# Optimization experiments

Hardware: AMD Instinct MI355X
Metric: run time of the kernel (lower is better)

The kernel has to match this reference:

```python
import jax, jax.numpy as jnp
import numpy as np
import math

B, N = 1, 512
C_S, C_Z, C_H, H, L, RECYCLE = 384, 128, 16, 12, 8, 2


def setup_inputs():
    key = jax.random.key(0)
    ks = jax.random.split(key, 16)
    w = lambda k, shape: jax.random.normal(k, shape, dtype=jnp.float32) * 0.02
    return {
        's': jax.random.normal(ks[0], (B, N, C_S), jnp.float32),
        'z': jax.random.normal(ks[1], (B, N, N, C_Z), jnp.float32),
        'Wq': w(ks[2], (L, C_S, H * C_H)), 'bq': jnp.zeros((L, H * C_H), jnp.float32),
        'Wk': w(ks[3], (L, C_S, H * C_H)), 'bk': jnp.zeros((L, H * C_H), jnp.float32),
        'Wv': w(ks[4], (L, C_S, H * C_H)), 'bv': jnp.zeros((L, H * C_H), jnp.float32),
        'Wb': w(ks[5], (L, C_Z, H)), 'bb': jnp.zeros((L, H), jnp.float32),
        'Wo': w(ks[6], (L, H * (C_H + C_Z), C_S)), 'bo': jnp.zeros((L, C_S), jnp.float32),
        'Wt1': w(ks[7], (L, C_S, 4 * C_S)), 'bt1': jnp.zeros((L, 4 * C_S), jnp.float32),
        'Wt2': w(ks[8], (L, 4 * C_S, C_S)), 'bt2': jnp.zeros((L, C_S), jnp.float32),
        'Wu': w(ks[9], (L, C_S, 6)), 'bu': jnp.zeros((L, 6), jnp.float32),
        'ln_g': jnp.ones((2 * L, C_S), jnp.float32),
        'ln_b': jnp.zeros((2 * L, C_S), jnp.float32),
    }


def _layer_norm(x, g, b, eps=1e-5):
    mu = jnp.mean(x, axis=-1, keepdims=True)
    var = jnp.mean((x - mu) ** 2, axis=-1, keepdims=True)
    return (x - mu) / jnp.sqrt(var + eps) * g + b


def _forward(s, z, Wq, bq, Wk, bk, Wv, bv, Wb, bb, Wo, bo, Wt1, bt1, Wt2, bt2, Wu, bu, ln_g, ln_b):
    b_, n_, _ = s.shape
    coords = jnp.zeros((b_, n_, 3), s.dtype)
    inv_sqrt_c = 1.0 / math.sqrt(C_H)
    for _r in range(RECYCLE):
        for i in range(L):
            # ---- Invariant Point Attention ----
            q = (s @ Wq[i] + bq[i]).reshape(b_, n_, H, C_H)
            k = (s @ Wk[i] + bk[i]).reshape(b_, n_, H, C_H)
            v = (s @ Wv[i] + bv[i]).reshape(b_, n_, H, C_H)
            attn = jnp.einsum('bihc,bjhc->bijh', q, k) * inv_sqrt_c  # (B,N,N,H)
            bias_z = z @ Wb[i] + bb[i]  # (B,N,N,H)
            # multiscale cdist bias: <=5A -> 1.0, <=15A -> 0.3, else 0.05
            sq = jnp.sum((coords[:, :, None, :] - coords[:, None, :, :]) ** 2, axis=-1)
            d = jnp.sqrt(jnp.maximum(sq, 1e-12))
            ms = jnp.where(d <= 5.0, 1.0, jnp.where(d <= 15.0, 0.3, 0.05))[..., None]
            attn = attn + bias_z + ms
            wgt = jax.nn.softmax(attn, axis=2)  # softmax over j
            scalar = jnp.einsum('bijh,bjhc->bihc', wgt, v)
            pair = jnp.einsum('bijh,bijc->bihc', wgt, z)
            o = jnp.concatenate([scalar, pair], axis=-1).reshape(b_, n_, H * (C_H + C_Z))
            s = _layer_norm(s + (o @ Wo[i] + bo[i]), ln_g[2 * i], ln_b[2 * i])
            # ---- Transition (FFN) ----
            t = jax.nn.relu(s @ Wt1[i] + bt1[i]) @ Wt2[i] + bt2[i]
            s = _layer_norm(s + t, ln_g[2 * i + 1], ln_b[2 * i + 1])
            # ---- Backbone update: source discards quaternion, applies translation only ----
            upd = s @ Wu[i] + bu[i]
            coords = coords + upd[..., :3]
    return coords


def reference(s, z, Wq, bq, Wk, bk, Wv, bv, Wb, bb, Wo, bo, Wt1, bt1, Wt2, bt2, Wu, bu, ln_g, ln_b):
    return _forward(s, z, Wq, bq, Wk, bk, Wv, bv, Wb, bb, Wo, bo, Wt1, bt1, Wt2, bt2, Wu, bu, ln_g, ln_b)
```

## Files before the change

### kernel.cpp

```cpp
#include <hip/hip_runtime.h>


constexpr int N    = 512;
constexpr int CS   = 384;
constexpr int CZ   = 128;
constexpr int CH   = 16;
constexpr int H    = 12;
constexpr int L    = 8;
constexpr int RECY = 2;
constexpr int HCH  = H * CH;
constexpr int QKVN = 3 * HCH;
constexpr int OD   = H * (CH + CZ);
constexpr int FF   = 4 * CS;
constexpr int MB   = 96;
constexpr long long NN2 = (long long)N * N;

typedef __bf16 bf16x8 __attribute__((ext_vector_type(8)));
typedef float  f32x4  __attribute__((ext_vector_type(4)));
typedef unsigned short us8 __attribute__((ext_vector_type(8)));

__device__ __forceinline__ ushort f2bf(float f) {
    uint u = __builtin_bit_cast(uint, f);
    return (ushort)((u + 0x7fffu + ((u >> 16) & 1u)) >> 16);
}
__device__ __forceinline__ float bf2f(ushort h) {
    uint u = ((uint)h) << 16;
    return __builtin_bit_cast(float, u);
}

__global__ __launch_bounds__(256) void init_s(
    const float* __restrict__ s_in, float* __restrict__ scur, ushort* __restrict__ sbf)
{
    int i = blockIdx.x * 256 + threadIdx.x;
    float v = s_in[i];
    scur[i] = v;
    sbf[i]  = f2bf(v);
}

__global__ __launch_bounds__(256) void pack_bqkv(
    const float* __restrict__ bq, const float* __restrict__ bk,
    const float* __restrict__ bv, float* __restrict__ bqkv)
{
    int idx = blockIdx.x * 256 + threadIdx.x;
    if (idx >= L * QKVN) return;
    int n = idx % QKVN, l = idx / QKVN;
    int sel = n / HCH, nn = n % HCH;
    const float* bp = sel == 0 ? bq : (sel == 1 ? bk : bv);
    bqkv[idx] = bp[l * HCH + nn];
}

__global__ __launch_bounds__(256) void pack_qkv_t(
    const float* __restrict__ Wq, const float* __restrict__ Wk,
    const float* __restrict__ Wv, ushort* __restrict__ WqkvT)
{
    __shared__ float tile[32][33];
    const int l = blockIdx.z;
    const int k0 = blockIdx.x * 32, n0 = blockIdx.y * 32;
    const int tx = threadIdx.x & 31, ty = threadIdx.x >> 5;
    const int sel = n0 / HCH;
    const int nn0 = n0 - sel * HCH;
    const float* W = sel == 0 ? Wq : (sel == 1 ? Wk : Wv);
    #pragma unroll
    for (int r = 0; r < 32; r += 8)
        tile[ty + r][tx] = W[((size_t)l * CS + k0 + ty + r) * HCH + nn0 + tx];
    __syncthreads();
    #pragma unroll
    for (int r = 0; r < 32; r += 8)
        WqkvT[((size_t)l * QKVN + n0 + ty + r) * CS + k0 + tx] = f2bf(tile[tx][ty + r]);
}

__global__ __launch_bounds__(256) void transpose_w(
    const float* __restrict__ in, ushort* __restrict__ out, int K, int Nn)
{
    __shared__ float tile[32][33];
    const int l = blockIdx.z;
    const float* ip = in + (size_t)l * K * Nn;
    ushort* op = out + (size_t)l * K * Nn;
    const int k0 = blockIdx.x * 32, n0 = blockIdx.y * 32;
    const int tx = threadIdx.x & 31, ty = threadIdx.x >> 5;
    #pragma unroll
    for (int r = 0; r < 32; r += 8)
        tile[ty + r][tx] = ip[(size_t)(k0 + ty + r) * Nn + n0 + tx];
    __syncthreads();
    #pragma unroll
    for (int r = 0; r < 32; r += 8)
        op[(size_t)(n0 + ty + r) * K + k0 + tx] = f2bf(tile[tx][ty + r]);
}

__global__ __launch_bounds__(256) void pack_wbt(
    const float* __restrict__ Wb, ushort* __restrict__ WbT)
{
    int idx = blockIdx.x * 256 + threadIdx.x;
    int m = idx >> 7, c = idx & 127;
    int l = m / H, h = m % H;
    WbT[idx] = f2bf(Wb[((size_t)l * CZ + c) * H + h]);
}

__global__ __launch_bounds__(256) void bias_gemm(
    const ushort* __restrict__ WbT, const float* __restrict__ z,
    const float* __restrict__ bb, ushort* __restrict__ bias_all)
{
    const int w = threadIdx.x >> 6, lane = threadIdx.x & 63;
    const int lm = lane & 15, kg = lane >> 4;
    const size_t ij0 = (size_t)blockIdx.x * 256 + (size_t)w * 64;
    __shared__ float bbs[MB];
    if (threadIdx.x < MB) bbs[threadIdx.x] = bb[threadIdx.x];
    __syncthreads();
    f32x4 acc[6][4];
    #pragma unroll
    for (int mt = 0; mt < 6; mt++)
        #pragma unroll
        for (int nt = 0; nt < 4; nt++) acc[mt][nt] = (f32x4){0.f, 0.f, 0.f, 0.f};
    #pragma unroll
    for (int kc = 0; kc < 4; kc++) {
        const int k = kc * 32 + kg * 8;
        bf16x8 b[4];
        #pragma unroll
        for (int nt = 0; nt < 4; nt++) {
            const float* zp = z + (ij0 + nt * 16 + lm) * CZ + k;
            float4 z0 = *(const float4*)zp, z1 = *(const float4*)(zp + 4);
            b[nt][0] = (__bf16)z0.x; b[nt][1] = (__bf16)z0.y;
            b[nt][2] = (__bf16)z0.z; b[nt][3] = (__bf16)z0.w;
            b[nt][4] = (__bf16)z1.x; b[nt][5] = (__bf16)z1.y;
            b[nt][6] = (__bf16)z1.z; b[nt][7] = (__bf16)z1.w;
        }
        #pragma unroll
        for (int mt = 0; mt < 6; mt++) {
            bf16x8 a = *(const bf16x8*)(WbT + (size_t)(mt * 16 + lm) * CZ + k);
            #pragma unroll
            for (int nt = 0; nt < 4; nt++)
                acc[mt][nt] = __builtin_amdgcn_mfma_f32_16x16x32_bf16(a, b[nt], acc[mt][nt], 0, 0, 0);
        }
    }
    #pragma unroll
    for (int mt = 0; mt < 6; mt++)
        #pragma unroll
        for (int nt = 0; nt < 4; nt++)
            #pragma unroll
            for (int r = 0; r < 4; r++) {
                int m = mt * 16 + kg * 4 + r;
                bias_all[(size_t)m * NN2 + ij0 + nt * 16 + lm] = f2bf(acc[mt][nt][r] + bbs[m]);
            }
}

__global__ __launch_bounds__(256) void gemm_bf16(
    const ushort* __restrict__ A, const ushort* __restrict__ Bt,
    const float* __restrict__ bias, float* __restrict__ C, ushort* __restrict__ Cbf,
    int M, int Nn, int K, int kper, int relu)
{
    const int w = threadIdx.x >> 6, lane = threadIdx.x & 63;
    const int lm = lane & 15, kg = lane >> 4;
    const int m0 = blockIdx.y * 64 + w * 16;
    const int n0 = blockIdx.x * 64;
    const int kbeg = blockIdx.z * kper;
    const ushort* Ap  = A  + (size_t)(m0 + lm) * K + kbeg + kg * 8;
    const ushort* Bp  = Bt + (size_t)(n0 + lm) * K + kbeg + kg * 8;
    f32x4 acc[4];
    #pragma unroll
    for (int ct = 0; ct < 4; ct++) acc[ct] = (f32x4){0.f, 0.f, 0.f, 0.f};
    for (int k = 0; k < kper; k += 32) {
        bf16x8 a = *(const bf16x8*)(Ap + k);
        #pragma unroll
        for (int ct = 0; ct < 4; ct++) {
            bf16x8 b = *(const bf16x8*)(Bp + (size_t)ct * 16 * K + k);
            acc[ct] = __builtin_amdgcn_mfma_f32_16x16x32_bf16(a, b, acc[ct], 0, 0, 0);
        }
    }
    float* Cz = C ? C + (size_t)blockIdx.z * M * Nn : nullptr;
    #pragma unroll
    for (int ct = 0; ct < 4; ct++) {
        int col = n0 + ct * 16 + lm;
        float bs = bias ? bias[col] : 0.f;
        #pragma unroll
        for (int r = 0; r < 4; r++) {
            int row = m0 + kg * 4 + r;
            float v = acc[ct][r] + bs;
            if (relu) v = fmaxf(v, 0.f);
            if (Cz)  Cz[(size_t)row * Nn + col] = v;
            if (Cbf) Cbf[(size_t)row * Nn + col] = f2bf(v);
        }
    }
}

__global__ __launch_bounds__(256) void v_transpose(
    const float* __restrict__ qkv, ushort* __restrict__ vT)
{
    __shared__ float tile[32][33];
    const int j0 = blockIdx.x * 32, p0 = blockIdx.y * 32;
    const int tx = threadIdx.x & 31, ty = threadIdx.x >> 5;
    #pragma unroll
    for (int r = 0; r < 32; r += 8)
        tile[ty + r][tx] = qkv[(size_t)(j0 + ty + r) * QKVN + 2 * HCH + p0 + tx];
    __syncthreads();
    #pragma unroll
    for (int r = 0; r < 32; r += 8)
        vT[(size_t)(p0 + ty + r) * N + j0 + tx] = f2bf(tile[tx][ty + r]);
}

__global__ __launch_bounds__(256) void attn_fused(
    const float* __restrict__ qkv, const ushort* __restrict__ bias_l,
    const float* __restrict__ coords, const ushort* __restrict__ z_t,
    const ushort* __restrict__ vT, ushort* __restrict__ obuf)
{
    const int i = blockIdx.x, t = threadIdx.x;
    const int w = t >> 6, lane = t & 63;
    const int lm = lane & 15, kg = lane >> 4;
    __shared__ float  qs[HCH];
    __shared__ float  cj[N * 3];
    __shared__ ushort wgt[16 * N];

    if (t < HCH) qs[t] = qkv[(size_t)i * QKVN + t] * 0.25f;
    #pragma unroll
    for (int e = 0; e < 6; e++) cj[e * 256 + t] = coords[e * 256 + t];
    __syncthreads();

    const float cix = cj[i * 3 + 0], ciy = cj[i * 3 + 1], ciz = cj[i * 3 + 2];
    const int j0 = lane * 8;
    const int slot_us = (lane >> 2) * 512 + (lane & 3) * 128;

    #pragma unroll
    for (int e = 0; e < 4; e++) {
        const int h = w + 4 * e;
        ushort* wp = wgt + slot_us + h * 8;
        if (e == 3) { us8 zz = {}; *(us8*)wp = zz; continue; }
        float lg[8];
        us8 bl = *(const us8*)(bias_l + (size_t)h * NN2 + (size_t)i * N + j0);
        #pragma unroll
        for (int jj = 0; jj < 8; jj++) {
            const int j = j0 + jj;
            const float4* kp = (const float4*)(qkv + (size_t)j * QKVN + HCH + h * CH);
            const float4* qp = (const float4*)(qs + h * CH);
            float d = 0.f;
            #pragma unroll
            for (int cq = 0; cq < 4; cq++) {
                float4 kv = kp[cq], qv = qp[cq];
                d += qv.x * kv.x + qv.y * kv.y + qv.z * kv.z + qv.w * kv.w;
            }
            float dx = cix - cj[j * 3 + 0];
            float dy = ciy - cj[j * 3 + 1];
            float dz = ciz - cj[j * 3 + 2];
            float d2 = dx * dx + dy * dy + dz * dz;
            float ms = d2 <= 25.f ? 1.f : (d2 <= 225.f ? 0.3f : 0.05f);
            lg[jj] = d + bf2f(bl[jj]) + ms;
        }
        float mx = lg[0];
        #pragma unroll
        for (int jj = 1; jj < 8; jj++) mx = fmaxf(mx, lg[jj]);
        #pragma unroll
        for (int off = 32; off > 0; off >>= 1) mx = fmaxf(mx, __shfl_xor(mx, off));
        float ex[8], sm = 0.f;
        #pragma unroll
        for (int jj = 0; jj < 8; jj++) { ex[jj] = __expf(lg[jj] - mx); sm += ex[jj]; }
        #pragma unroll
        for (int off = 32; off > 0; off >>= 1) sm += __shfl_xor(sm, off);
        const float inv = 1.f / sm;
        us8 wv;
        #pragma unroll
        for (int jj = 0; jj < 8; jj++) wv[jj] = f2bf(ex[jj] * inv);
        *(us8*)wp = wv;
    }
    __syncthreads();

    const ushort* Bz = z_t + (size_t)i * CZ * N;
    f32x4 ap[2], as_[3];
    ap[0] = ap[1] = (f32x4){0.f, 0.f, 0.f, 0.f};
    as_[0] = as_[1] = as_[2] = (f32x4){0.f, 0.f, 0.f, 0.f};
    const int cbase = w * 32;
    const int pbase = 3 * w * 16;
    for (int kk = 0; kk < 16; kk++) {
        bf16x8 a = *(const bf16x8*)(wgt + kk * 512 + lane * 8);
        const int ko = kk * 32 + kg * 8;
        #pragma unroll
        for (int ntl = 0; ntl < 2; ntl++) {
            bf16x8 b = *(const bf16x8*)(Bz + (size_t)(cbase + ntl * 16 + lm) * N + ko);
            ap[ntl] = __builtin_amdgcn_mfma_f32_16x16x32_bf16(a, b, ap[ntl], 0, 0, 0);
        }
        #pragma unroll
        for (int si = 0; si < 3; si++) {
            bf16x8 b = *(const bf16x8*)(vT + (size_t)(pbase + si * 16 + lm) * N + ko);
            as_[si] = __builtin_amdgcn_mfma_f32_16x16x32_bf16(a, b, as_[si], 0, 0, 0);
        }
    }
    const size_t ob = (size_t)i * OD;
    if (kg < 3) {
        #pragma unroll
        for (int ntl = 0; ntl < 2; ntl++)
            #pragma unroll
            for (int r = 0; r < 4; r++) {
                int h = kg * 4 + r;
                obuf[ob + h * 144 + 16 + cbase + ntl * 16 + lm] = f2bf(ap[ntl][r]);
            }
    }
    #pragma unroll
    for (int si = 0; si < 3; si++) {
        int ht = 3 * w + si;
        if (kg == (ht >> 2)) obuf[ob + ht * 144 + lm] = f2bf(as_[si][ht & 3]);
    }
}

__global__ __launch_bounds__(128) void ln_residual(
    const float* __restrict__ x, int parts, const float* __restrict__ gb,
    float* __restrict__ s, ushort* __restrict__ sbf,
    const float* __restrict__ g, const float* __restrict__ b,
    const float* __restrict__ Wu_l, const float* __restrict__ bu_l,
    float* __restrict__ coords)
{
    const int i = blockIdx.x, t = threadIdx.x;
    __shared__ float red[4];
    __shared__ float redc[2][3];
    float v[3];
    float sum = 0.f;
    #pragma unroll
    for (int e = 0; e < 3; e++) {
        int c = t + e * 128;
        float a = s[(size_t)i * CS + c] + gb[c];
        for (int p = 0; p < parts; p++) a += x[(size_t)p * N * CS + (size_t)i * CS + c];
        v[e] = a; sum += a;
    }
    #pragma unroll
    for (int off = 32; off > 0; off >>= 1) sum += __shfl_down(sum, off);
    if ((t & 63) == 0) red[t >> 6] = sum;
    __syncthreads();
    float mu = (red[0] + red[1]) * (1.f / CS);
    float vs = 0.f;
    #pragma unroll
    for (int e = 0; e < 3; e++) { float d = v[e] - mu; vs += d * d; }
    #pragma unroll
    for (int off = 32; off > 0; off >>= 1) vs += __shfl_down(vs, off);
    if ((t & 63) == 0) red[2 + (t >> 6)] = vs;
    __syncthreads();
    float inv = rsqrtf((red[2] + red[3]) * (1.f / CS) + 1e-5f);
    float a0 = 0.f, a1 = 0.f, a2 = 0.f;
    #pragma unroll
    for (int e = 0; e < 3; e++) {
        int c = t + e * 128;
        float ov = (v[e] - mu) * inv * g[c] + b[c];
        s[(size_t)i * CS + c]   = ov;
        sbf[(size_t)i * CS + c] = f2bf(ov);
        if (Wu_l) {
            a0 += ov * Wu_l[c * 6 + 0];
            a1 += ov * Wu_l[c * 6 + 1];
            a2 += ov * Wu_l[c * 6 + 2];
        }
    }
    if (Wu_l) {
        #pragma unroll
        for (int off = 32; off > 0; off >>= 1) {
            a0 += __shfl_down(a0, off);
            a1 += __shfl_down(a1, off);
            a2 += __shfl_down(a2, off);
        }
        if ((t & 63) == 0) {
            redc[t >> 6][0] = a0; redc[t >> 6][1] = a1; redc[t >> 6][2] = a2;
        }
        __syncthreads();
        if (t == 0) {
            coords[i * 3 + 0] += redc[0][0] + redc[1][0] + bu_l[0];
            coords[i * 3 + 1] += redc[0][1] + redc[1][1] + bu_l[1];
            coords[i * 3 + 2] += redc[0][2] + redc[1][2] + bu_l[2];
        }
    }
}

extern "C" void kernel_launch(void* const* d_in, const int* in_sizes, int n_in,
                              void* d_out, int out_size, void* d_ws, size_t ws_size,
                              hipStream_t stream)
{
    const float* s_in = (const float*)d_in[0];
    const float* z    = (const float*)d_in[1];
    const float* Wq   = (const float*)d_in[2];
    const float* bq   = (const float*)d_in[3];
    const float* Wk   = (const float*)d_in[4];
    const float* bk   = (const float*)d_in[5];
    const float* Wv   = (const float*)d_in[6];
    const float* bv   = (const float*)d_in[7];
    const float* Wb   = (const float*)d_in[8];
    const float* bb   = (const float*)d_in[9];
    const float* Wo   = (const float*)d_in[10];
    const float* bo   = (const float*)d_in[11];
    const float* Wt1  = (const float*)d_in[12];
    const float* bt1  = (const float*)d_in[13];
    const float* Wt2  = (const float*)d_in[14];
    const float* bt2  = (const float*)d_in[15];
    const float* Wu   = (const float*)d_in[16];
    const float* bu   = (const float*)d_in[17];
    const float* lng  = (const float*)d_in[18];
    const float* lnb  = (const float*)d_in[19];
    float* coords = (float*)d_out;

    float* wsf   = (float*)d_ws;
    float* qkv   = wsf;
    float* tmp2  = qkv + (size_t)N * QKVN;
    float* scur  = tmp2 + (size_t)9 * N * CS;
    float* bqkv  = scur + (size_t)N * CS;
    ushort* wsu     = (ushort*)(bqkv + (size_t)L * QKVN);
    ushort* bias_all= wsu;
    ushort* z_t     = bias_all + (size_t)MB * NN2;
    ushort* WqkvT   = z_t + (size_t)N * CZ * N;
    ushort* WoT     = WqkvT + (size_t)L * CS * QKVN;
    ushort* Wt1T    = WoT + (size_t)L * OD * CS;
    ushort* Wt2T    = Wt1T + (size_t)L * CS * FF;
    ushort* WbT     = Wt2T + (size_t)L * FF * CS;
    ushort* vT      = WbT + (size_t)MB * CZ;
    ushort* scur_bf = vT + (size_t)HCH * N;
    ushort* obuf_bf = scur_bf + (size_t)N * CS;
    ushort* tmp1_bf = obuf_bf + (size_t)N * OD;
    (void)in_sizes; (void)n_in; (void)out_size; (void)ws_size;

    hipMemsetAsync(coords, 0, (size_t)N * 3 * sizeof(float), stream);
    init_s<<<(N * CS) / 256, 256, 0, stream>>>(s_in, scur, scur_bf);
    pack_bqkv<<<(L * QKVN + 255) / 256, 256, 0, stream>>>(bq, bk, bv, bqkv);
    pack_qkv_t<<<dim3(CS / 32, QKVN / 32, L), 256, 0, stream>>>(Wq, Wk, Wv, WqkvT);
    transpose_w<<<dim3(OD / 32, CS / 32, L), 256, 0, stream>>>(Wo, WoT, OD, CS);
    transpose_w<<<dim3(CS / 32, FF / 32, L), 256, 0, stream>>>(Wt1, Wt1T, CS, FF);
    transpose_w<<<dim3(FF / 32, CS / 32, L), 256, 0, stream>>>(Wt2, Wt2T, FF, CS);
    transpose_w<<<dim3(N / 32, CZ / 32, N), 256, 0, stream>>>(z, z_t, N, CZ);
    pack_wbt<<<(MB * CZ) / 256, 256, 0, stream>>>(Wb, WbT);
    bias_gemm<<<(int)(NN2 / 256), 256, 0, stream>>>(WbT, z, bb, bias_all);

    for (int r = 0; r < RECY; r++) {
        for (int l = 0; l < L; l++) {
            gemm_bf16<<<dim3(QKVN / 64, N / 64, 1), 256, 0, stream>>>(
                scur_bf, WqkvT + (size_t)l * CS * QKVN, bqkv + l * QKVN,
                qkv, nullptr, N, QKVN, CS, CS, 0);
            v_transpose<<<dim3(N / 32, HCH / 32), 256, 0, stream>>>(qkv, vT);
            attn_fused<<<N, 256, 0, stream>>>(
                qkv, bias_all + (size_t)l * H * NN2, coords, z_t, vT, obuf_bf);
            gemm_bf16<<<dim3(CS / 64, N / 64, 9), 256, 0, stream>>>(
                obuf_bf, WoT + (size_t)l * OD * CS, nullptr,
                tmp2, nullptr, N, CS, OD, OD / 9, 0);
            ln_residual<<<N, 128, 0, stream>>>(
                tmp2, 9, bo + l * CS, scur, scur_bf,
                lng + (size_t)(2 * l) * CS, lnb + (size_t)(2 * l) * CS,
                nullptr, nullptr, nullptr);
            gemm_bf16<<<dim3(FF / 64, N / 64, 1), 256, 0, stream>>>(
                scur_bf, Wt1T + (size_t)l * CS * FF, bt1 + l * FF,
                nullptr, tmp1_bf, N, FF, CS, CS, 1);
            gemm_bf16<<<dim3(CS / 64, N / 64, 8), 256, 0, stream>>>(
                tmp1_bf, Wt2T + (size_t)l * FF * CS, nullptr,
                tmp2, nullptr, N, CS, FF, FF / 8, 0);
            ln_residual<<<N, 128, 0, stream>>>(
                tmp2, 8, bt2 + l * CS, scur, scur_bf,
                lng + (size_t)(2 * l + 1) * CS, lnb + (size_t)(2 * l + 1) * CS,
                Wu + (size_t)l * CS * 6, bu + l * 6, coords);
        }
    }
}
```

Baseline: 2.443 ms.

## Fuse V transpose into QKV GEMM, split K accumulators, template LN parts

Writes the transposed bf16 V directly from the QKV GEMM epilogue, which removes the separate v_transpose kernel launch per layer. The GEMM inner loop now splits K into two halves with independent accumulators, giving more loads and MFMAs in flight. It also unrolls the attention PV loop by two and makes the LayerNorm partial-sum count a template parameter. The split-K halves require kper to be a multiple of 64, and the extra accumulators raise register use.

```diff
diff --git a/kernel.cpp b/kernel.cpp
--- a/kernel.cpp
+++ b/kernel.cpp
@@ -146,6 +146,7 @@
 __global__ __launch_bounds__(256) void gemm_bf16(
     const ushort* __restrict__ A, const ushort* __restrict__ Bt,
     const float* __restrict__ bias, float* __restrict__ C, ushort* __restrict__ Cbf,
+    ushort* __restrict__ vTout,
     int M, int Nn, int K, int kper, int relu)
 {
     const int w = threadIdx.x >> 6, lane = threadIdx.x & 63;
@@ -153,17 +154,24 @@
     const int m0 = blockIdx.y * 64 + w * 16;
     const int n0 = blockIdx.x * 64;
     const int kbeg = blockIdx.z * kper;
+    const int kh = kper >> 1;
     const ushort* Ap  = A  + (size_t)(m0 + lm) * K + kbeg + kg * 8;
     const ushort* Bp  = Bt + (size_t)(n0 + lm) * K + kbeg + kg * 8;
-    f32x4 acc[4];
-    #pragma unroll
-    for (int ct = 0; ct < 4; ct++) acc[ct] = (f32x4){0.f, 0.f, 0.f, 0.f};
-    for (int k = 0; k < kper; k += 32) {
-        bf16x8 a = *(const bf16x8*)(Ap + k);
+    f32x4 acc[4], ac2[4];
+    #pragma unroll
+    for (int ct = 0; ct < 4; ct++) {
+        acc[ct] = (f32x4){0.f, 0.f, 0.f, 0.f};
+        ac2[ct] = (f32x4){0.f, 0.f, 0.f, 0.f};
+    }
+    for (int k = 0; k < kh; k += 32) {
+        bf16x8 a0 = *(const bf16x8*)(Ap + k);
+        bf16x8 a1 = *(const bf16x8*)(Ap + kh + k);
         #pragma unroll
         for (int ct = 0; ct < 4; ct++) {
-            bf16x8 b = *(const bf16x8*)(Bp + (size_t)ct * 16 * K + k);
-            acc[ct] = __builtin_amdgcn_mfma_f32_16x16x32_bf16(a, b, acc[ct], 0, 0, 0);
+            bf16x8 b0 = *(const bf16x8*)(Bp + (size_t)ct * 16 * K + k);
+            bf16x8 b1 = *(const bf16x8*)(Bp + (size_t)ct * 16 * K + kh + k);
+            acc[ct] = __builtin_amdgcn_mfma_f32_16x16x32_bf16(a0, b0, acc[ct], 0, 0, 0);
+            ac2[ct] = __builtin_amdgcn_mfma_f32_16x16x32_bf16(a1, b1, ac2[ct], 0, 0, 0);
         }
     }
     float* Cz = C ? C + (size_t)blockIdx.z * M * Nn : nullptr;
@@ -171,30 +179,22 @@
     for (int ct = 0; ct < 4; ct++) {
         int col = n0 + ct * 16 + lm;
         float bs = bias ? bias[col] : 0.f;
+        float vv[4];
         #pragma unroll
         for (int r = 0; r < 4; r++) {
             int row = m0 + kg * 4 + r;
-            float v = acc[ct][r] + bs;
+            float v = acc[ct][r] + ac2[ct][r] + bs;
             if (relu) v = fmaxf(v, 0.f);
+            vv[r] = v;
             if (Cz)  Cz[(size_t)row * Nn + col] = v;
             if (Cbf) Cbf[(size_t)row * Nn + col] = f2bf(v);
         }
-    }
-}
-
-__global__ __launch_bounds__(256) void v_transpose(
-    const float* __restrict__ qkv, ushort* __restrict__ vT)
-{
-    __shared__ float tile[32][33];
-    const int j0 = blockIdx.x * 32, p0 = blockIdx.y * 32;
-    const int tx = threadIdx.x & 31, ty = threadIdx.x >> 5;
-    #pragma unroll
-    for (int r = 0; r < 32; r += 8)
-        tile[ty + r][tx] = qkv[(size_t)(j0 + ty + r) * QKVN + 2 * HCH + p0 + tx];
-    __syncthreads();
-    #pragma unroll
-    for (int r = 0; r < 32; r += 8)
-        vT[(size_t)(p0 + ty + r) * N + j0 + tx] = f2bf(tile[tx][ty + r]);
+        if (vTout && col >= 2 * HCH) {
+            ushort4 o;
+            o.x = f2bf(vv[0]); o.y = f2bf(vv[1]); o.z = f2bf(vv[2]); o.w = f2bf(vv[3]);
+            *(ushort4*)(vTout + (size_t)(col - 2 * HCH) * N + m0 + kg * 4) = o;
+        }
+    }
 }
 
 __global__ __launch_bounds__(256) void attn_fused(
@@ -267,6 +267,7 @@
     as_[0] = as_[1] = as_[2] = (f32x4){0.f, 0.f, 0.f, 0.f};
     const int cbase = w * 32;
     const int pbase = 3 * w * 16;
+    #pragma unroll 2
     for (int kk = 0; kk < 16; kk++) {
         bf16x8 a = *(const bf16x8*)(wgt + kk * 512 + lane * 8);
         const int ko = kk * 32 + kg * 8;
@@ -298,8 +299,9 @@
     }
 }
 
+template<int PARTS>
 __global__ __launch_bounds__(128) void ln_residual(
-    const float* __restrict__ x, int parts, const float* __restrict__ gb,
+    const float* __restrict__ x, const float* __restrict__ gb,
     float* __restrict__ s, ushort* __restrict__ sbf,
     const float* __restrict__ g, const float* __restrict__ b,
     const float* __restrict__ Wu_l, const float* __restrict__ bu_l,
@@ -314,7 +316,8 @@
     for (int e = 0; e < 3; e++) {
         int c = t + e * 128;
         float a = s[(size_t)i * CS + c] + gb[c];
-        for (int p = 0; p < parts; p++) a += x[(size_t)p * N * CS + (size_t)i * CS + c];
+        #pragma unroll
+        for (int p = 0; p < PARTS; p++) a += x[(size_t)p * N * CS + (size_t)i * CS + c];
         v[e] = a; sum += a;
     }
     #pragma unroll
@@ -422,25 +425,24 @@
         for (int l = 0; l < L; l++) {
             gemm_bf16<<<dim3(QKVN / 64, N / 64, 1), 256, 0, stream>>>(
                 scur_bf, WqkvT + (size_t)l * CS * QKVN, bqkv + l * QKVN,
-                qkv, nullptr, N, QKVN, CS, CS, 0);
-            v_transpose<<<dim3(N / 32, HCH / 32), 256, 0, stream>>>(qkv, vT);
+                qkv, nullptr, vT, N, QKVN, CS, CS, 0);
             attn_fused<<<N, 256, 0, stream>>>(
                 qkv, bias_all + (size_t)l * H * NN2, coords, z_t, vT, obuf_bf);
             gemm_bf16<<<dim3(CS / 64, N / 64, 9), 256, 0, stream>>>(
                 obuf_bf, WoT + (size_t)l * OD * CS, nullptr,
-                tmp2, nullptr, N, CS, OD, OD / 9, 0);
-            ln_residual<<<N, 128, 0, stream>>>(
-                tmp2, 9, bo + l * CS, scur, scur_bf,
+                tmp2, nullptr, nullptr, N, CS, OD, OD / 9, 0);
+            ln_residual<9><<<N, 128, 0, stream>>>(
+                tmp2, bo + l * CS, scur, scur_bf,
                 lng + (size_t)(2 * l) * CS, lnb + (size_t)(2 * l) * CS,
                 nullptr, nullptr, nullptr);
             gemm_bf16<<<dim3(FF / 64, N / 64, 1), 256, 0, stream>>>(
                 scur_bf, Wt1T + (size_t)l * CS * FF, bt1 + l * FF,
-                nullptr, tmp1_bf, N, FF, CS, CS, 1);
+                nullptr, tmp1_bf, nullptr, N, FF, CS, CS, 1);
             gemm_bf16<<<dim3(CS / 64, N / 64, 8), 256, 0, stream>>>(
                 tmp1_bf, Wt2T + (size_t)l * FF * CS, nullptr,
-                tmp2, nullptr, N, CS, FF, FF / 8, 0);
-            ln_residual<<<N, 128, 0, stream>>>(
-                tmp2, 8, bt2 + l * CS, scur, scur_bf,
+                tmp2, nullptr, nullptr, N, CS, FF, FF / 8, 0);
+            ln_residual<8><<<N, 128, 0, stream>>>(
+                tmp2, bt2 + l * CS, scur, scur_bf,
                 lng + (size_t)(2 * l + 1) * CS, lnb + (size_t)(2 * l + 1) * CS,
                 Wu + (size_t)l * CS * 6, bu + l * 6, coords);
         }
```

Result: faster. 2.069 ms (-15.3%).
